# Kernel optimization log

Hardware: AMD Instinct MI355X
Metric: run time of the kernel (lower is better)

The kernel has to match this reference:

```python
import jax, jax.numpy as jnp
import numpy as np

B, NFIELD, NEMB, NFILTER, NLAYERS = 256, 64, 64, 128, 3


def setup_inputs() -> dict:
    key = jax.random.key(0)
    ks = jax.random.split(key, 5)
    x = jax.random.normal(ks[0], (B, NFIELD, NEMB), dtype=jnp.float32)
    # Conv1d(k=1, bias=False) weights, squeezed to (out_ch, in_ch). Small init for stability.
    W0 = jax.random.normal(ks[1], (NFILTER, NFIELD * NFIELD), dtype=jnp.float32) * 0.02
    W1 = jax.random.normal(ks[2], (NFILTER, NFIELD * NFILTER), dtype=jnp.float32) * 0.02
    W2 = jax.random.normal(ks[3], (NFILTER, NFIELD * NFILTER), dtype=jnp.float32) * 0.02
    Wa = jax.random.normal(ks[4], (1, NLAYERS * NFILTER), dtype=jnp.float32) * 0.02
    return {"x": x, "W0": W0, "W1": W1, "W2": W2, "Wa": Wa}


def reference(x, W0, W1, W2, Wa):
    # x: (B, F, E). CIN recurrence over a fixed small number of layers.
    Ws = [W0, W1, W2]
    x0 = x
    xk = x
    pooled = []
    for W in Ws:
        # outer product over field axes: (B, F, C, E)
        h = x0[:, :, None, :] * xk[:, None, :, :]
        b, f, c, e = h.shape
        h = h.reshape(b, f * c, e)
        # 1x1 conv == GEMM over channel dim, then ReLU
        xk = jax.nn.relu(jnp.einsum('oc,bce->boe', W, h))
        # sum-pool over embedding dim: (B, nfilter)
        pooled.append(jnp.sum(xk, axis=-1))
    feats = jnp.concatenate(pooled, axis=1)  # (B, nlayers*nfilter)
    y = feats @ Wa.T                         # (B, 1)
    return y[:, 0]
```

## Files before the change

### kernel.cpp

```cpp
#include <hip/hip_runtime.h>

#define NBATCH 256

typedef __attribute__((ext_vector_type(8))) short bf16x8;
typedef __attribute__((ext_vector_type(4))) float f32x4;

__device__ __forceinline__ unsigned short f2b(float f) {
    unsigned u = __float_as_uint(f);
    u = (u + 0x7fffu + ((u >> 16) & 1u)) >> 16;
    return (unsigned short)u;
}
__device__ __forceinline__ float b2f(unsigned short h) {
    return __uint_as_float(((unsigned)h) << 16);
}
__device__ __forceinline__ void async16(const void* g, void* l) {
    __builtin_amdgcn_global_load_lds((const __attribute__((address_space(1))) unsigned int*)g,
                                     (__attribute__((address_space(3))) unsigned int*)l, 16, 0, 0);
}

__global__ void prep_all(const float* __restrict__ x,
                         const float* __restrict__ W0,
                         const float* __restrict__ W1,
                         const float* __restrict__ W2,
                         unsigned short* __restrict__ x0t,
                         unsigned short* __restrict__ x0f,
                         unsigned short* __restrict__ Wp0,
                         unsigned short* __restrict__ Wp1,
                         unsigned short* __restrict__ Wp2)
{
    const int bid = blockIdx.x, tid = threadIdx.x;
    if (bid < 2560) {
        const float* W; unsigned short* Wp; int CLOG, KLOG, lbid;
        if (bid < 512)       { W = W0; Wp = Wp0; CLOG = 6; KLOG = 12; lbid = bid; }
        else if (bid < 1536) { W = W1; Wp = Wp1; CLOG = 7; KLOG = 13; lbid = bid - 512; }
        else                 { W = W2; Wp = Wp2; CLOG = 7; KLOG = 13; lbid = bid - 1536; }
        const int base = (lbid * 256 + tid) * 4;
        int o = base >> KLOG, k = base & ((1 << KLOG) - 1);
        int f = k >> CLOG, c = k & ((1 << CLOG) - 1);
        int rg = o >> 4, l15 = o & 15;
        int cs = c >> 5, kseg = (c >> 3) & 3, j = c & 7;
        int NCS = 1 << (CLOG - 5);
        int NK = 64 * NCS;
        int kstep = f * NCS + cs;
        size_t dst = (((size_t)rg * NK + kstep) * 64 + kseg * 16 + l15) * 8 + j;
        const float4 wv = *(const float4*)(W + base);
        ushort4 ov = make_ushort4(f2b(wv.x), f2b(wv.y), f2b(wv.z), f2b(wv.w));
        *(ushort4*)(Wp + dst) = ov;
    } else {
        const int base = ((bid - 2560) * 256 + tid) * 4;
        int b = base >> 12, r = base & 4095, f = r >> 6, e0 = r & 63;
        const float4 xv = *(const float4*)(x + base);
        ushort4 v = make_ushort4(f2b(xv.x), f2b(xv.y), f2b(xv.z), f2b(xv.w));
        *(ushort4*)(x0f + b * 4096 + f * 64 + e0) = v;
        x0t[b * 4096 + (e0 + 0) * 64 + f] = v.x;
        x0t[b * 4096 + (e0 + 1) * 64 + f] = v.y;
        x0t[b * 4096 + (e0 + 2) * 64 + f] = v.z;
        x0t[b * 4096 + (e0 + 3) * 64 + f] = v.w;
    }
}

template <int CL, bool LAST>
__global__ __launch_bounds__(512, 1) void layer_k(
    const unsigned short* __restrict__ Wp,
    const unsigned short* __restrict__ Bsrc,
    const unsigned short* __restrict__ x0f,
    const float* __restrict__ Wa_l,
    unsigned short* __restrict__ xknext,
    float* __restrict__ ybuf)
{
    constexpr int NCS = CL / 32;
    constexpr int NK  = 64 * NCS;
    constexpr int NCH = NK / 16;
    constexpr int NFOLD = 16 / NCS;
    extern __shared__ char sm[];
    char* smA = sm;
    char* smX = sm + 32768;
    const int bid = blockIdx.x, tid = threadIdx.x;
    const int rg = bid & 7, sg = bid >> 3;
    const int lane = tid & 63, w = tid >> 6;
    const int l15 = lane & 15, kseg = lane >> 4;
    const int b = sg * 8 + w;

    {
        const char* src = (const char*)x0f + (size_t)b * 8192 + lane * 16;
        char* dst = smX + w * 8192;
#pragma unroll
        for (int i = 0; i < 8; ++i) async16(src + i * 1024, dst + i * 1024);
    }

    bf16x8 bq[NCS][4];
    {
        const char* Bb = (const char*)Bsrc + (size_t)b * (CL * 128) + kseg * 16;
#pragma unroll
        for (int cs = 0; cs < NCS; ++cs)
#pragma unroll
            for (int nt = 0; nt < 4; ++nt)
                bq[cs][nt] = *(const bf16x8*)(Bb + (nt * 16 + l15) * (CL * 2) + cs * 64);
    }

    const char* Ab = (const char*)Wp + (size_t)rg * NK * 1024;
    auto stage = [&](int ch, int buf) {
        const char* src = Ab + (size_t)ch * 16384 + w * 2048 + lane * 16;
        char* dst = smA + buf * 16384 + w * 2048;
        async16(src, dst);
        async16(src + 1024, dst + 1024);
    };
    stage(0, 0);
    __syncthreads();

    const unsigned short* XF = (const unsigned short*)(smX + w * 8192);
    const f32x4 ZERO = {0.f, 0.f, 0.f, 0.f};
    f32x4 acc[4], accf[4];
#pragma unroll
    for (int nt = 0; nt < 4; ++nt) acc[nt] = ZERO;

    for (int ch = 0; ch < NCH; ++ch) {
        const int cur = ch & 1;
        if (ch + 1 < NCH) stage(ch + 1, cur ^ 1);
#pragma unroll
        for (int cs = 0; cs < NCS; ++cs)
            asm volatile("" :: "v"(bq[cs][0]), "v"(bq[cs][1]), "v"(bq[cs][2]), "v"(bq[cs][3]));
        const char* Abuf = smA + cur * 16384 + lane * 16;
#pragma unroll
        for (int gi = 0; gi < NFOLD; ++gi) {
            const int fg = ch * NFOLD + gi;
            const float sv0 = b2f(XF[fg * 64 + l15]);
            const float sv1 = b2f(XF[fg * 64 + 16 + l15]);
            const float sv2 = b2f(XF[fg * 64 + 32 + l15]);
            const float sv3 = b2f(XF[fg * 64 + 48 + l15]);
#pragma unroll
            for (int cs = 0; cs < NCS; ++cs) {
                const bf16x8 a = *(const bf16x8*)(Abuf + (gi * NCS + cs) * 1024);
#pragma unroll
                for (int nt = 0; nt < 4; ++nt)
                    accf[nt] = __builtin_amdgcn_mfma_f32_16x16x32_bf16(
                        a, bq[cs][nt], (cs == 0) ? ZERO : accf[nt], 0, 0, 0);
            }
            acc[0] += accf[0] * sv0;
            acc[1] += accf[1] * sv1;
            acc[2] += accf[2] * sv2;
            acc[3] += accf[3] * sv3;
        }
        __syncthreads();
    }

    const float4 wa = *(const float4*)(Wa_l + rg * 16 + kseg * 4);
    float ypart = 0.f;
#pragma unroll
    for (int nt = 0; nt < 4; ++nt) {
        f32x4 v = acc[nt];
        v.x = fmaxf(v.x, 0.f); v.y = fmaxf(v.y, 0.f);
        v.z = fmaxf(v.z, 0.f); v.w = fmaxf(v.w, 0.f);
        ypart = fmaf(wa.x, v.x, ypart);
        ypart = fmaf(wa.y, v.y, ypart);
        ypart = fmaf(wa.z, v.z, ypart);
        ypart = fmaf(wa.w, v.w, ypart);
        if (!LAST) {
            unsigned lo = (unsigned)f2b(v.x) | ((unsigned)f2b(v.y) << 16);
            unsigned hi = (unsigned)f2b(v.z) | ((unsigned)f2b(v.w) << 16);
            *(uint2*)((char*)xknext + (size_t)b * 16384 + (nt * 16 + l15) * 256
                      + (rg * 16 + kseg * 4) * 2) = make_uint2(lo, hi);
        }
    }
#pragma unroll
    for (int off = 32; off >= 1; off >>= 1)
        ypart += __shfl_down(ypart, off, 64);
    if (lane == 0) ybuf[b * 8 + rg] = ypart;
}

__global__ void finalize_k(const float* __restrict__ ybuf, float* __restrict__ y) {
    const int b = threadIdx.x;
    float s = 0.f;
#pragma unroll
    for (int l = 0; l < 3; ++l)
#pragma unroll
        for (int r = 0; r < 8; ++r)
            s += ybuf[l * 2048 + b * 8 + r];
    y[b] = s;
}

extern "C" void kernel_launch(void* const* d_in, const int* in_sizes, int n_in,
                              void* d_out, int out_size, void* d_ws, size_t ws_size,
                              hipStream_t stream) {
    const float* x  = (const float*)d_in[0];
    const float* W0 = (const float*)d_in[1];
    const float* W1 = (const float*)d_in[2];
    const float* W2 = (const float*)d_in[3];
    const float* Wa = (const float*)d_in[4];
    float* y = (float*)d_out;

    char* ws = (char*)d_ws;
    unsigned short* Wp0  = (unsigned short*)(ws + 0x000000);
    unsigned short* Wp1  = (unsigned short*)(ws + 0x110000);
    unsigned short* Wp2  = (unsigned short*)(ws + 0x320000);
    unsigned short* x0t  = (unsigned short*)(ws + 0x530000);
    unsigned short* x0f  = (unsigned short*)(ws + 0x730000);
    unsigned short* xkA  = (unsigned short*)(ws + 0x930000);
    unsigned short* xkB  = (unsigned short*)(ws + 0xD30000);
    float*          ybuf = (float*)(ws + 0x1130000);

    hipLaunchKernelGGL(prep_all, dim3(3584), dim3(256), 0, stream,
                       x, W0, W1, W2, x0t, x0f, Wp0, Wp1, Wp2);

    hipFuncSetAttribute((const void*)layer_k<64, false>,
                        hipFuncAttributeMaxDynamicSharedMemorySize, 98304);
    hipFuncSetAttribute((const void*)layer_k<128, false>,
                        hipFuncAttributeMaxDynamicSharedMemorySize, 98304);
    hipFuncSetAttribute((const void*)layer_k<128, true>,
                        hipFuncAttributeMaxDynamicSharedMemorySize, 98304);

    hipLaunchKernelGGL((layer_k<64, false>), dim3(256), dim3(512), 98304, stream,
                       Wp0, x0t, x0f, Wa + 0, xkA, ybuf + 0);
    hipLaunchKernelGGL((layer_k<128, false>), dim3(256), dim3(512), 98304, stream,
                       Wp1, xkA, x0f, Wa + 128, xkB, ybuf + 2048);
    hipLaunchKernelGGL((layer_k<128, true>), dim3(256), dim3(512), 98304, stream,
                       Wp2, xkB, x0f, Wa + 256, xkA, ybuf + 4096);

    hipLaunchKernelGGL(finalize_k, dim3(1), dim3(256), 0, stream, ybuf, y);
}
```

Baseline: 100.3 us.

## Switch CIN layers to 32x32x16 MFMA with split-K across waves

The weight packing and layer kernel move from 16x16x32 to 32x32x16 bf16 MFMA tiles. Each block now covers 32 output channels for 4 samples, and the field (K) dimension is split across two wave groups whose partial sums are reduced through LDS. Launch bounds allow 2 blocks per CU and the A staging buffer grows to 32KB per stage. The aim is fewer accumulator scaling ops per MFMA and better operand reuse, at the cost of an extra LDS reduction step, a sync, and more register pressure.

```diff
diff --git a/kernel.cpp b/kernel.cpp
--- a/kernel.cpp
+++ b/kernel.cpp
@@ -2,8 +2,8 @@
 
 #define NBATCH 256
 
-typedef __attribute__((ext_vector_type(8))) short bf16x8;
-typedef __attribute__((ext_vector_type(4))) float f32x4;
+typedef __attribute__((ext_vector_type(8)))  short bf16x8;
+typedef __attribute__((ext_vector_type(16))) float f32x16;
 
 __device__ __forceinline__ unsigned short f2b(float f) {
     unsigned u = __float_as_uint(f);
@@ -35,17 +35,16 @@
         else if (bid < 1536) { W = W1; Wp = Wp1; CLOG = 7; KLOG = 13; lbid = bid - 512; }
         else                 { W = W2; Wp = Wp2; CLOG = 7; KLOG = 13; lbid = bid - 1536; }
         const int base = (lbid * 256 + tid) * 4;
+        const int NKL = 1 << (KLOG - 4);
         int o = base >> KLOG, k = base & ((1 << KLOG) - 1);
         int f = k >> CLOG, c = k & ((1 << CLOG) - 1);
-        int rg = o >> 4, l15 = o & 15;
-        int cs = c >> 5, kseg = (c >> 3) & 3, j = c & 7;
-        int NCS = 1 << (CLOG - 5);
-        int NK = 64 * NCS;
-        int kstep = f * NCS + cs;
-        size_t dst = (((size_t)rg * NK + kstep) * 64 + kseg * 16 + l15) * 8 + j;
+        int rgg = o >> 5;
+        int lane = (o & 31) + ((c >> 3) & 1) * 32;
+        int kstep = f * (1 << (CLOG - 4)) + (c >> 4);
+        int j0 = c & 7;
+        size_t dst = (((size_t)rgg * NKL + kstep) * 64 + lane) * 8 + j0;
         const float4 wv = *(const float4*)(W + base);
-        ushort4 ov = make_ushort4(f2b(wv.x), f2b(wv.y), f2b(wv.z), f2b(wv.w));
-        *(ushort4*)(Wp + dst) = ov;
+        *(ushort4*)(Wp + dst) = make_ushort4(f2b(wv.x), f2b(wv.y), f2b(wv.z), f2b(wv.w));
     } else {
         const int base = ((bid - 2560) * 256 + tid) * 4;
         int b = base >> 12, r = base & 4095, f = r >> 6, e0 = r & 63;
@@ -60,7 +59,7 @@
 }
 
 template <int CL, bool LAST>
-__global__ __launch_bounds__(512, 1) void layer_k(
+__global__ __launch_bounds__(512, 2) void layer_k(
     const unsigned short* __restrict__ Wp,
     const unsigned short* __restrict__ Bsrc,
     const unsigned short* __restrict__ x0f,
@@ -68,115 +67,139 @@
     unsigned short* __restrict__ xknext,
     float* __restrict__ ybuf)
 {
-    constexpr int NCS = CL / 32;
-    constexpr int NK  = 64 * NCS;
-    constexpr int NCH = NK / 16;
-    constexpr int NFOLD = 16 / NCS;
+    constexpr int NCS16 = CL / 16;
+    constexpr int NK    = 64 * NCS16;
+    constexpr int NKg   = NK / 2;
+    constexpr int NCH   = NKg / 16;
+    constexpr int FPC   = 16 / NCS16;
     extern __shared__ char sm[];
     char* smA = sm;
-    char* smX = sm + 32768;
+    char* smX = sm + 65536;
+
     const int bid = blockIdx.x, tid = threadIdx.x;
-    const int rg = bid & 7, sg = bid >> 3;
+    const int rgg = bid & 3, sgg = bid >> 2;
     const int lane = tid & 63, w = tid >> 6;
-    const int l15 = lane & 15, kseg = lane >> 4;
-    const int b = sg * 8 + w;
-
+    const int p = w & 3, kg = w >> 2;
+    const int s = sgg * 4 + p;
+    const int l31 = lane & 31, khalf = lane >> 5;
+
+#pragma unroll
+    for (int q = 0; q < 4; ++q)
+        async16((const char*)x0f + (size_t)(sgg * 4 + q) * 8192 + tid * 16,
+                smX + q * 8192 + w * 1024);
+
+    bf16x8 bq[NCS16][2];
     {
-        const char* src = (const char*)x0f + (size_t)b * 8192 + lane * 16;
-        char* dst = smX + w * 8192;
-#pragma unroll
-        for (int i = 0; i < 8; ++i) async16(src + i * 1024, dst + i * 1024);
-    }
-
-    bf16x8 bq[NCS][4];
-    {
-        const char* Bb = (const char*)Bsrc + (size_t)b * (CL * 128) + kseg * 16;
-#pragma unroll
-        for (int cs = 0; cs < NCS; ++cs)
-#pragma unroll
-            for (int nt = 0; nt < 4; ++nt)
-                bq[cs][nt] = *(const bf16x8*)(Bb + (nt * 16 + l15) * (CL * 2) + cs * 64);
-    }
-
-    const char* Ab = (const char*)Wp + (size_t)rg * NK * 1024;
+        const char* Bb = (const char*)Bsrc + ((size_t)s * 64 + l31) * (CL * 2) + khalf * 16;
+#pragma unroll
+        for (int cs = 0; cs < NCS16; ++cs)
+#pragma unroll
+            for (int t = 0; t < 2; ++t)
+                bq[cs][t] = *(const bf16x8*)(Bb + t * 32 * (CL * 2) + cs * 32);
+    }
+
+    const char* Ab = (const char*)Wp + (size_t)rgg * NK * 1024;
     auto stage = [&](int ch, int buf) {
-        const char* src = Ab + (size_t)ch * 16384 + w * 2048 + lane * 16;
-        char* dst = smA + buf * 16384 + w * 2048;
-        async16(src, dst);
-        async16(src + 1024, dst + 1024);
+#pragma unroll
+        for (int i = 0; i < 4; ++i) {
+            const int g = i * 8 + w;
+            const int ksg = (i < 2) ? (ch * 16 + g) : (NKg + ch * 16 + (g - 16));
+            async16(Ab + (size_t)ksg * 1024 + lane * 16,
+                    smA + buf * 32768 + g * 1024);
+        }
     };
     stage(0, 0);
     __syncthreads();
 
-    const unsigned short* XF = (const unsigned short*)(smX + w * 8192);
-    const f32x4 ZERO = {0.f, 0.f, 0.f, 0.f};
-    f32x4 acc[4], accf[4];
-#pragma unroll
-    for (int nt = 0; nt < 4; ++nt) acc[nt] = ZERO;
+    const unsigned short* XS = (const unsigned short*)(smX + p * 8192);
+    const f32x16 ZERO = {0.f};
+    f32x16 acc[2] = {ZERO, ZERO};
+    f32x16 ae[2], ao[2];
 
     for (int ch = 0; ch < NCH; ++ch) {
         const int cur = ch & 1;
         if (ch + 1 < NCH) stage(ch + 1, cur ^ 1);
 #pragma unroll
-        for (int cs = 0; cs < NCS; ++cs)
-            asm volatile("" :: "v"(bq[cs][0]), "v"(bq[cs][1]), "v"(bq[cs][2]), "v"(bq[cs][3]));
-        const char* Abuf = smA + cur * 16384 + lane * 16;
-#pragma unroll
-        for (int gi = 0; gi < NFOLD; ++gi) {
-            const int fg = ch * NFOLD + gi;
-            const float sv0 = b2f(XF[fg * 64 + l15]);
-            const float sv1 = b2f(XF[fg * 64 + 16 + l15]);
-            const float sv2 = b2f(XF[fg * 64 + 32 + l15]);
-            const float sv3 = b2f(XF[fg * 64 + 48 + l15]);
-#pragma unroll
-            for (int cs = 0; cs < NCS; ++cs) {
-                const bf16x8 a = *(const bf16x8*)(Abuf + (gi * NCS + cs) * 1024);
-#pragma unroll
-                for (int nt = 0; nt < 4; ++nt)
-                    accf[nt] = __builtin_amdgcn_mfma_f32_16x16x32_bf16(
-                        a, bq[cs][nt], (cs == 0) ? ZERO : accf[nt], 0, 0, 0);
+        for (int cs = 0; cs < NCS16; ++cs)
+            asm volatile("" :: "v"(bq[cs][0]), "v"(bq[cs][1]));
+        const char* Abuf = smA + cur * 32768 + kg * 16384 + lane * 16;
+#pragma unroll
+        for (int fi = 0; fi < FPC; ++fi) {
+            const int fg = kg * 32 + ch * FPC + fi;
+            const float sv0 = b2f(XS[fg * 64 + l31]);
+            const float sv1 = b2f(XS[fg * 64 + 32 + l31]);
+#pragma unroll
+            for (int cs = 0; cs < NCS16; ++cs) {
+                const bf16x8 a = *(const bf16x8*)(Abuf + (fi * NCS16 + cs) * 1024);
+                if ((cs & 1) == 0) {
+                    ae[0] = __builtin_amdgcn_mfma_f32_32x32x16_bf16(a, bq[cs][0], (cs == 0) ? ZERO : ae[0], 0, 0, 0);
+                    ae[1] = __builtin_amdgcn_mfma_f32_32x32x16_bf16(a, bq[cs][1], (cs == 0) ? ZERO : ae[1], 0, 0, 0);
+                } else {
+                    ao[0] = __builtin_amdgcn_mfma_f32_32x32x16_bf16(a, bq[cs][0], (cs == 1) ? ZERO : ao[0], 0, 0, 0);
+                    ao[1] = __builtin_amdgcn_mfma_f32_32x32x16_bf16(a, bq[cs][1], (cs == 1) ? ZERO : ao[1], 0, 0, 0);
+                }
             }
-            acc[0] += accf[0] * sv0;
-            acc[1] += accf[1] * sv1;
-            acc[2] += accf[2] * sv2;
-            acc[3] += accf[3] * sv3;
+#pragma unroll
+            for (int t = 0; t < 2; ++t) {
+                const f32x16 sf = (t == 0)
+                    ? f32x16{sv0,sv0,sv0,sv0,sv0,sv0,sv0,sv0,sv0,sv0,sv0,sv0,sv0,sv0,sv0,sv0}
+                    : f32x16{sv1,sv1,sv1,sv1,sv1,sv1,sv1,sv1,sv1,sv1,sv1,sv1,sv1,sv1,sv1,sv1};
+                acc[t] += (ae[t] + ao[t]) * sf;
+            }
         }
         __syncthreads();
     }
 
-    const float4 wa = *(const float4*)(Wa_l + rg * 16 + kseg * 4);
-    float ypart = 0.f;
-#pragma unroll
-    for (int nt = 0; nt < 4; ++nt) {
-        f32x4 v = acc[nt];
-        v.x = fmaxf(v.x, 0.f); v.y = fmaxf(v.y, 0.f);
-        v.z = fmaxf(v.z, 0.f); v.w = fmaxf(v.w, 0.f);
-        ypart = fmaf(wa.x, v.x, ypart);
-        ypart = fmaf(wa.y, v.y, ypart);
-        ypart = fmaf(wa.z, v.z, ypart);
-        ypart = fmaf(wa.w, v.w, ypart);
-        if (!LAST) {
-            unsigned lo = (unsigned)f2b(v.x) | ((unsigned)f2b(v.y) << 16);
-            unsigned hi = (unsigned)f2b(v.z) | ((unsigned)f2b(v.w) << 16);
-            *(uint2*)((char*)xknext + (size_t)b * 16384 + (nt * 16 + l15) * 256
-                      + (rg * 16 + kseg * 4) * 2) = make_uint2(lo, hi);
+    if (kg == 1) {
+#pragma unroll
+        for (int t = 0; t < 2; ++t)
+            *(f32x16*)(smA + p * 8192 + lane * 128 + t * 64) = acc[t];
+    }
+    __syncthreads();
+    if (kg == 0) {
+#pragma unroll
+        for (int t = 0; t < 2; ++t)
+            acc[t] += *(const f32x16*)(smA + p * 8192 + lane * 128 + t * 64);
+
+        float ypart = 0.f;
+#pragma unroll
+        for (int t = 0; t < 2; ++t) {
+            const int ecol = l31 + t * 32;
+#pragma unroll
+            for (int q = 0; q < 4; ++q) {
+                const int o0 = rgg * 32 + 8 * q + 4 * khalf;
+                float v0 = fmaxf(acc[t][q * 4 + 0], 0.f);
+                float v1 = fmaxf(acc[t][q * 4 + 1], 0.f);
+                float v2 = fmaxf(acc[t][q * 4 + 2], 0.f);
+                float v3 = fmaxf(acc[t][q * 4 + 3], 0.f);
+                ypart = fmaf(Wa_l[o0 + 0], v0, ypart);
+                ypart = fmaf(Wa_l[o0 + 1], v1, ypart);
+                ypart = fmaf(Wa_l[o0 + 2], v2, ypart);
+                ypart = fmaf(Wa_l[o0 + 3], v3, ypart);
+                if (!LAST) {
+                    unsigned lo = (unsigned)f2b(v0) | ((unsigned)f2b(v1) << 16);
+                    unsigned hi = (unsigned)f2b(v2) | ((unsigned)f2b(v3) << 16);
+                    *(uint2*)((char*)xknext + (((size_t)s * 64 + ecol) * 128 + o0) * 2)
+                        = make_uint2(lo, hi);
+                }
+            }
         }
-    }
-#pragma unroll
-    for (int off = 32; off >= 1; off >>= 1)
-        ypart += __shfl_down(ypart, off, 64);
-    if (lane == 0) ybuf[b * 8 + rg] = ypart;
+#pragma unroll
+        for (int off = 32; off >= 1; off >>= 1)
+            ypart += __shfl_down(ypart, off, 64);
+        if (lane == 0) ybuf[s * 4 + rgg] = ypart;
+    }
 }
 
 __global__ void finalize_k(const float* __restrict__ ybuf, float* __restrict__ y) {
     const int b = threadIdx.x;
-    float s = 0.f;
+    float sum = 0.f;
 #pragma unroll
     for (int l = 0; l < 3; ++l)
 #pragma unroll
-        for (int r = 0; r < 8; ++r)
-            s += ybuf[l * 2048 + b * 8 + r];
-    y[b] = s;
+        for (int r = 0; r < 4; ++r)
+            sum += ybuf[l * 1024 + b * 4 + r];
+    y[b] = sum;
 }
 
 extern "C" void kernel_launch(void* const* d_in, const int* in_sizes, int n_in,
@@ -212,9 +235,9 @@
     hipLaunchKernelGGL((layer_k<64, false>), dim3(256), dim3(512), 98304, stream,
                        Wp0, x0t, x0f, Wa + 0, xkA, ybuf + 0);
     hipLaunchKernelGGL((layer_k<128, false>), dim3(256), dim3(512), 98304, stream,
-                       Wp1, xkA, x0f, Wa + 128, xkB, ybuf + 2048);
+                       Wp1, xkA, x0f, Wa + 128, xkB, ybuf + 1024);
     hipLaunchKernelGGL((layer_k<128, true>), dim3(256), dim3(512), 98304, stream,
-                       Wp2, xkB, x0f, Wa + 256, xkA, ybuf + 4096);
+                       Wp2, xkB, x0f, Wa + 256, xkA, ybuf + 2048);
 
     hipLaunchKernelGGL(finalize_k, dim3(1), dim3(256), 0, stream, ybuf, y);
 }
```

Result: slower. 108.8 us (+8.5%).

## Split K across wave pairs, stream A from global to registers, double grid

Applied to the files above, without the earlier changes.

Each block now covers 4 samples instead of 8. Its 8 waves split the channel (K) reduction into two halves, and the partial accumulators are combined through shared memory at the end. The weight tiles are loaded straight from global memory into double-buffered registers, replacing the LDS staging and the per-chunk barrier. The grid doubles to 512 blocks with launch bounds of 2 blocks per SM and 48KB of static LDS, aiming for more occupancy and fewer syncs. The trade-off is more global and L2 traffic for the weights, since each wave reads A itself, plus an extra reduction step.

```diff
diff --git a/kernel.cpp b/kernel.cpp
--- a/kernel.cpp
+++ b/kernel.cpp
@@ -44,8 +44,7 @@
         int kstep = f * NCS + cs;
         size_t dst = (((size_t)rg * NK + kstep) * 64 + kseg * 16 + l15) * 8 + j;
         const float4 wv = *(const float4*)(W + base);
-        ushort4 ov = make_ushort4(f2b(wv.x), f2b(wv.y), f2b(wv.z), f2b(wv.w));
-        *(ushort4*)(Wp + dst) = ov;
+        *(ushort4*)(Wp + dst) = make_ushort4(f2b(wv.x), f2b(wv.y), f2b(wv.z), f2b(wv.w));
     } else {
         const int base = ((bid - 2560) * 256 + tid) * 4;
         int b = base >> 12, r = base & 4095, f = r >> 6, e0 = r & 63;
@@ -60,7 +59,7 @@
 }
 
 template <int CL, bool LAST>
-__global__ __launch_bounds__(512, 1) void layer_k(
+__global__ __launch_bounds__(512, 2) void layer_k(
     const unsigned short* __restrict__ Wp,
     const unsigned short* __restrict__ Bsrc,
     const unsigned short* __restrict__ x0f,
@@ -68,115 +67,130 @@
     unsigned short* __restrict__ xknext,
     float* __restrict__ ybuf)
 {
-    constexpr int NCS = CL / 32;
-    constexpr int NK  = 64 * NCS;
-    constexpr int NCH = NK / 16;
-    constexpr int NFOLD = 16 / NCS;
-    extern __shared__ char sm[];
-    char* smA = sm;
-    char* smX = sm + 32768;
+    constexpr int NCS  = CL / 32;
+    constexpr int NCS2 = NCS / 2;
+    constexpr int NK   = 64 * NCS;
+    __shared__ char sm[49152];
+    char* smX = sm;
+    char* smR = sm + 32768;
+
     const int bid = blockIdx.x, tid = threadIdx.x;
-    const int rg = bid & 7, sg = bid >> 3;
+    const int rg = bid & 7, sgg = bid >> 3;
     const int lane = tid & 63, w = tid >> 6;
+    const int p = w & 3, kg = w >> 2;
+    const int s = sgg * 4 + p;
     const int l15 = lane & 15, kseg = lane >> 4;
-    const int b = sg * 8 + w;
-
+
+#pragma unroll
+    for (int q = 0; q < 4; ++q)
+        async16((const char*)x0f + (size_t)(sgg * 4 + q) * 8192 + w * 1024 + lane * 16,
+                smX + q * 8192 + w * 1024);
+
+    bf16x8 bq[NCS2][4];
     {
-        const char* src = (const char*)x0f + (size_t)b * 8192 + lane * 16;
-        char* dst = smX + w * 8192;
-#pragma unroll
-        for (int i = 0; i < 8; ++i) async16(src + i * 1024, dst + i * 1024);
-    }
-
-    bf16x8 bq[NCS][4];
-    {
-        const char* Bb = (const char*)Bsrc + (size_t)b * (CL * 128) + kseg * 16;
-#pragma unroll
-        for (int cs = 0; cs < NCS; ++cs)
+        const char* Bb = (const char*)Bsrc + (size_t)s * (CL * 128) + kseg * 16;
+#pragma unroll
+        for (int i = 0; i < NCS2; ++i)
 #pragma unroll
             for (int nt = 0; nt < 4; ++nt)
-                bq[cs][nt] = *(const bf16x8*)(Bb + (nt * 16 + l15) * (CL * 2) + cs * 64);
-    }
-
-    const char* Ab = (const char*)Wp + (size_t)rg * NK * 1024;
-    auto stage = [&](int ch, int buf) {
-        const char* src = Ab + (size_t)ch * 16384 + w * 2048 + lane * 16;
-        char* dst = smA + buf * 16384 + w * 2048;
-        async16(src, dst);
-        async16(src + 1024, dst + 1024);
-    };
-    stage(0, 0);
+                bq[i][nt] = *(const bf16x8*)(Bb + (nt * 16 + l15) * (CL * 2)
+                                             + (kg * NCS2 + i) * 64);
+    }
+
+    const char* Ag = (const char*)Wp + (size_t)rg * NK * 1024 + (kseg * 16 + l15) * 16;
+#define LD_A(dst, f) { _Pragma("unroll") for (int i_ = 0; i_ < NCS2; ++i_) \
+    dst[i_] = *(const bf16x8*)(Ag + (size_t)((f) * NCS + kg * NCS2 + i_) * 1024); }
+
+    bf16x8 aqA[NCS2], aqB[NCS2];
+    LD_A(aqA, 0);
+
     __syncthreads();
 
-    const unsigned short* XF = (const unsigned short*)(smX + w * 8192);
+    const unsigned short* XS = (const unsigned short*)(smX + p * 8192);
     const f32x4 ZERO = {0.f, 0.f, 0.f, 0.f};
     f32x4 acc[4], accf[4];
 #pragma unroll
     for (int nt = 0; nt < 4; ++nt) acc[nt] = ZERO;
 
-    for (int ch = 0; ch < NCH; ++ch) {
-        const int cur = ch & 1;
-        if (ch + 1 < NCH) stage(ch + 1, cur ^ 1);
-#pragma unroll
-        for (int cs = 0; cs < NCS; ++cs)
-            asm volatile("" :: "v"(bq[cs][0]), "v"(bq[cs][1]), "v"(bq[cs][2]), "v"(bq[cs][3]));
-        const char* Abuf = smA + cur * 16384 + lane * 16;
-#pragma unroll
-        for (int gi = 0; gi < NFOLD; ++gi) {
-            const int fg = ch * NFOLD + gi;
-            const float sv0 = b2f(XF[fg * 64 + l15]);
-            const float sv1 = b2f(XF[fg * 64 + 16 + l15]);
-            const float sv2 = b2f(XF[fg * 64 + 32 + l15]);
-            const float sv3 = b2f(XF[fg * 64 + 48 + l15]);
-#pragma unroll
-            for (int cs = 0; cs < NCS; ++cs) {
-                const bf16x8 a = *(const bf16x8*)(Abuf + (gi * NCS + cs) * 1024);
-#pragma unroll
-                for (int nt = 0; nt < 4; ++nt)
-                    accf[nt] = __builtin_amdgcn_mfma_f32_16x16x32_bf16(
-                        a, bq[cs][nt], (cs == 0) ? ZERO : accf[nt], 0, 0, 0);
+#define CONSUME(A, f) { \
+    const float sv0 = b2f(XS[(f) * 64 + l15]); \
+    const float sv1 = b2f(XS[(f) * 64 + 16 + l15]); \
+    const float sv2 = b2f(XS[(f) * 64 + 32 + l15]); \
+    const float sv3 = b2f(XS[(f) * 64 + 48 + l15]); \
+    _Pragma("unroll") for (int i_ = 0; i_ < NCS2; ++i_) { \
+        _Pragma("unroll") for (int nt_ = 0; nt_ < 4; ++nt_) \
+            accf[nt_] = __builtin_amdgcn_mfma_f32_16x16x32_bf16( \
+                A[i_], bq[i_][nt_], (i_ == 0) ? ZERO : accf[nt_], 0, 0, 0); \
+    } \
+    acc[0] += accf[0] * f32x4{sv0, sv0, sv0, sv0}; \
+    acc[1] += accf[1] * f32x4{sv1, sv1, sv1, sv1}; \
+    acc[2] += accf[2] * f32x4{sv2, sv2, sv2, sv2}; \
+    acc[3] += accf[3] * f32x4{sv3, sv3, sv3, sv3}; }
+
+    for (int ch = 0; ch < 8; ++ch) {
+#pragma unroll
+        for (int i = 0; i < NCS2; ++i)
+            asm volatile("" :: "v"(bq[i][0]), "v"(bq[i][1]), "v"(bq[i][2]), "v"(bq[i][3]));
+#pragma unroll
+        for (int fi = 0; fi < 8; ++fi) {
+            const int f = ch * 8 + fi;
+            if ((fi & 1) == 0) {
+                LD_A(aqB, f + 1);
+                CONSUME(aqA, f);
+            } else {
+                if (f < 63) LD_A(aqA, f + 1);
+                CONSUME(aqB, f);
             }
-            acc[0] += accf[0] * sv0;
-            acc[1] += accf[1] * sv1;
-            acc[2] += accf[2] * sv2;
-            acc[3] += accf[3] * sv3;
         }
-        __syncthreads();
-    }
-
-    const float4 wa = *(const float4*)(Wa_l + rg * 16 + kseg * 4);
-    float ypart = 0.f;
-#pragma unroll
-    for (int nt = 0; nt < 4; ++nt) {
-        f32x4 v = acc[nt];
-        v.x = fmaxf(v.x, 0.f); v.y = fmaxf(v.y, 0.f);
-        v.z = fmaxf(v.z, 0.f); v.w = fmaxf(v.w, 0.f);
-        ypart = fmaf(wa.x, v.x, ypart);
-        ypart = fmaf(wa.y, v.y, ypart);
-        ypart = fmaf(wa.z, v.z, ypart);
-        ypart = fmaf(wa.w, v.w, ypart);
-        if (!LAST) {
-            unsigned lo = (unsigned)f2b(v.x) | ((unsigned)f2b(v.y) << 16);
-            unsigned hi = (unsigned)f2b(v.z) | ((unsigned)f2b(v.w) << 16);
-            *(uint2*)((char*)xknext + (size_t)b * 16384 + (nt * 16 + l15) * 256
-                      + (rg * 16 + kseg * 4) * 2) = make_uint2(lo, hi);
+    }
+#undef LD_A
+#undef CONSUME
+
+    if (kg == 1) {
+#pragma unroll
+        for (int nt = 0; nt < 4; ++nt)
+            *(f32x4*)(smR + p * 4096 + lane * 64 + nt * 16) = acc[nt];
+    }
+    __syncthreads();
+    if (kg == 0) {
+#pragma unroll
+        for (int nt = 0; nt < 4; ++nt)
+            acc[nt] += *(const f32x4*)(smR + p * 4096 + lane * 64 + nt * 16);
+
+        const float4 wa = *(const float4*)(Wa_l + rg * 16 + kseg * 4);
+        float ypart = 0.f;
+#pragma unroll
+        for (int nt = 0; nt < 4; ++nt) {
+            f32x4 v = acc[nt];
+            v.x = fmaxf(v.x, 0.f); v.y = fmaxf(v.y, 0.f);
+            v.z = fmaxf(v.z, 0.f); v.w = fmaxf(v.w, 0.f);
+            ypart = fmaf(wa.x, v.x, ypart);
+            ypart = fmaf(wa.y, v.y, ypart);
+            ypart = fmaf(wa.z, v.z, ypart);
+            ypart = fmaf(wa.w, v.w, ypart);
+            if (!LAST) {
+                unsigned lo = (unsigned)f2b(v.x) | ((unsigned)f2b(v.y) << 16);
+                unsigned hi = (unsigned)f2b(v.z) | ((unsigned)f2b(v.w) << 16);
+                *(uint2*)((char*)xknext + (size_t)s * 16384 + (nt * 16 + l15) * 256
+                          + (rg * 16 + kseg * 4) * 2) = make_uint2(lo, hi);
+            }
         }
-    }
-#pragma unroll
-    for (int off = 32; off >= 1; off >>= 1)
-        ypart += __shfl_down(ypart, off, 64);
-    if (lane == 0) ybuf[b * 8 + rg] = ypart;
+#pragma unroll
+        for (int off = 32; off >= 1; off >>= 1)
+            ypart += __shfl_down(ypart, off, 64);
+        if (lane == 0) ybuf[s * 8 + rg] = ypart;
+    }
 }
 
 __global__ void finalize_k(const float* __restrict__ ybuf, float* __restrict__ y) {
     const int b = threadIdx.x;
-    float s = 0.f;
+    float sum = 0.f;
 #pragma unroll
     for (int l = 0; l < 3; ++l)
 #pragma unroll
         for (int r = 0; r < 8; ++r)
-            s += ybuf[l * 2048 + b * 8 + r];
-    y[b] = s;
+            sum += ybuf[l * 2048 + b * 8 + r];
+    y[b] = sum;
 }
 
 extern "C" void kernel_launch(void* const* d_in, const int* in_sizes, int n_in,
@@ -202,18 +216,11 @@
     hipLaunchKernelGGL(prep_all, dim3(3584), dim3(256), 0, stream,
                        x, W0, W1, W2, x0t, x0f, Wp0, Wp1, Wp2);
 
-    hipFuncSetAttribute((const void*)layer_k<64, false>,
-                        hipFuncAttributeMaxDynamicSharedMemorySize, 98304);
-    hipFuncSetAttribute((const void*)layer_k<128, false>,
-                        hipFuncAttributeMaxDynamicSharedMemorySize, 98304);
-    hipFuncSetAttribute((const void*)layer_k<128, true>,
-                        hipFuncAttributeMaxDynamicSharedMemorySize, 98304);
-
-    hipLaunchKernelGGL((layer_k<64, false>), dim3(256), dim3(512), 98304, stream,
+    hipLaunchKernelGGL((layer_k<64, false>), dim3(512), dim3(512), 0, stream,
                        Wp0, x0t, x0f, Wa + 0, xkA, ybuf + 0);
-    hipLaunchKernelGGL((layer_k<128, false>), dim3(256), dim3(512), 98304, stream,
+    hipLaunchKernelGGL((layer_k<128, false>), dim3(512), dim3(512), 0, stream,
                        Wp1, xkA, x0f, Wa + 128, xkB, ybuf + 2048);
-    hipLaunchKernelGGL((layer_k<128, true>), dim3(256), dim3(512), 98304, stream,
+    hipLaunchKernelGGL((layer_k<128, true>), dim3(512), dim3(512), 0, stream,
                        Wp2, xkB, x0f, Wa + 256, xkA, ybuf + 4096);
 
     hipLaunchKernelGGL(finalize_k, dim3(1), dim3(256), 0, stream, ybuf, y);
```

Result: slower. 109.5 us (+9.2%).
